# Kernel optimization log

Hardware: AMD Instinct MI355X
Metric: run time of the kernel (lower is better)

## Reference

```python
import jax, jax.numpy as jnp
import numpy as np

B, T, D, H, TE = 8, 1024, 1024, 16, 2048  # batch, seq, latent_dim, heads, time_embed_dim
LN_EPS = 1e-5


def layer_norm(x, w, b):
    m = jnp.mean(x, axis=-1, keepdims=True)
    v = jnp.var(x, axis=-1, keepdims=True)
    return (x - m) / jnp.sqrt(v + LN_EPS) * w + b


def setup_inputs() -> dict:
    key = jax.random.key(0)
    ks = jax.random.split(key, 8)
    s = lambda k, sh: (jax.random.normal(k, sh, jnp.float32) * 0.02)
    return dict(
        x=jax.random.normal(ks[0], (B, T, D), jnp.float32),
        emb=jax.random.normal(ks[1], (B, TE), jnp.float32),
        src_mask=jnp.ones((B, T), jnp.float32),
        norm_w=jnp.ones((D,), jnp.float32), norm_b=jnp.zeros((D,), jnp.float32),
        q_w=s(ks[2], (D, D)), q_b=jnp.zeros((D,), jnp.float32),
        k_w=s(ks[3], (D, D)), k_b=jnp.zeros((D,), jnp.float32),
        v_w=s(ks[4], (D, D)), v_b=jnp.zeros((D,), jnp.float32),
        emb_w=s(ks[5], (TE, 2 * D)), emb_b=jnp.zeros((2 * D,), jnp.float32),
        sb_norm_w=jnp.ones((D,), jnp.float32), sb_norm_b=jnp.zeros((D,), jnp.float32),
        out_w=s(ks[6], (D, D)), out_b=jnp.zeros((D,), jnp.float32),
    )


def reference(x, emb, src_mask, norm_w, norm_b, q_w, q_b, k_w, k_b, v_w, v_b,
              emb_w, emb_b, sb_norm_w, sb_norm_b, out_w, out_b):
    Bx, Tx, Dx = x.shape
    # the torch module applies the SAME LayerNorm to x three times; compute once
    xn = layer_norm(x, norm_w, norm_b)                      # [B,T,D]
    q = (xn @ q_w + q_b).reshape(Bx, Tx, H, -1)             # [B,T,H,l]
    k = (xn @ k_w + k_b).reshape(Bx, Tx, H, -1)
    att = jnp.einsum('bnhl,bmhl->bnmh', q, k)               # [B,T,T,H] (no 1/sqrt(d) scaling, as in source)
    mask = src_mask.reshape(Bx, 1, Tx, 1)
    att = att + (1.0 - mask) * -1000000.0
    att = jax.nn.softmax(att, axis=2)                       # softmax over keys (dim m)
    v = ((xn @ v_w + v_b) * src_mask[:, :, None]).reshape(Bx, Tx, H, -1)
    y = jnp.einsum('bnmh,bmhl->bnhl', att, v).reshape(Bx, Tx, Dx)
    # StylizationBlock (dropout is identity in eval)
    e = jax.nn.silu(emb) @ emb_w + emb_b                    # [B,2D]
    scale, shift = jnp.split(e[:, None, :], 2, axis=2)      # each [B,1,D]
    h = layer_norm(y, sb_norm_w, sb_norm_b) * (1.0 + scale) + shift
    h = jax.nn.silu(h) @ out_w + out_b
    return x + h
```

## Files before the change

### kernel.cpp

```cpp
#include <hip/hip_runtime.h>
#include <cstddef>
#include <cstdint>

#define B_SZ 8
#define T_SEQ 1024
#define D_MODEL 1024
#define NH 16
#define HD 64
#define TE_DIM 2048
#define BT_ROWS 8192

typedef short bf16x8 __attribute__((ext_vector_type(8)));
typedef float f32x4 __attribute__((ext_vector_type(4)));

#define MFMA16(a, b, c) __builtin_amdgcn_mfma_f32_16x16x32_bf16(a, b, c, 0, 0, 0)
#define EXP2(x) __builtin_amdgcn_exp2f(x)

__device__ inline unsigned short f2b(float f) {
  union { float f; unsigned u; } v; v.f = f;
  unsigned r = v.u + 0x7FFF + ((v.u >> 16) & 1);
  return (unsigned short)(r >> 16);
}

__device__ inline float b2f(unsigned short u) {
  union { unsigned u; float f; } v; v.u = ((unsigned)u) << 16; return v.f;
}

__device__ inline unsigned cvtpk(float a, float b) {
  unsigned r;
  asm("v_cvt_pk_bf16_f32 %0, %1, %2" : "=v"(r) : "v"(a), "v"(b));
  return r;
}

__device__ inline void gll16(const void* g, void* l) {
  __builtin_amdgcn_global_load_lds(
      (const __attribute__((address_space(1))) unsigned int*)g,
      (__attribute__((address_space(3))) unsigned int*)l, 16, 0, 0);
}

__global__ __launch_bounds__(256) void ln_kernel(
    const float* __restrict__ x, const float* __restrict__ w,
    const float* __restrict__ b, unsigned short* __restrict__ out)
{
  __shared__ float red[8];
  int row = blockIdx.x;
  int tid = threadIdx.x;
  const float* xr = x + (size_t)row * D_MODEL;
  float4 xv = *(const float4*)&xr[tid * 4];
  float s  = xv.x + xv.y + xv.z + xv.w;
  float ss = xv.x*xv.x + xv.y*xv.y + xv.z*xv.z + xv.w*xv.w;
  #pragma unroll
  for (int off = 32; off; off >>= 1) {
    s  += __shfl_xor(s, off);
    ss += __shfl_xor(ss, off);
  }
  int wv = tid >> 6;
  if ((tid & 63) == 0) { red[wv] = s; red[4 + wv] = ss; }
  __syncthreads();
  s  = red[0] + red[1] + red[2] + red[3];
  ss = red[4] + red[5] + red[6] + red[7];
  float mean = s * (1.f / D_MODEL);
  float var  = ss * (1.f / D_MODEL) - mean * mean;
  float inv  = rsqrtf(var + 1e-5f);
  float4 w4 = *(const float4*)&w[tid * 4];
  float4 b4 = *(const float4*)&b[tid * 4];
  ushort4 o;
  o.x = f2b((xv.x - mean) * inv * w4.x + b4.x);
  o.y = f2b((xv.y - mean) * inv * w4.y + b4.y);
  o.z = f2b((xv.z - mean) * inv * w4.z + b4.z);
  o.w = f2b((xv.w - mean) * inv * w4.w + b4.w);
  int kg = tid >> 4, cb = (tid >> 1) & 7, e = (tid & 1) * 4;
  int col = kg * 64 + ((cb ^ (row & 7)) * 8) + e;
  *(ushort4*)&out[(size_t)row * D_MODEL + col] = o;
}

__global__ __launch_bounds__(256) void transpose_w4(
    const float* __restrict__ s0, const float* __restrict__ s1,
    const float* __restrict__ s2, const float* __restrict__ s3,
    unsigned short* __restrict__ d0, unsigned short* __restrict__ d1,
    unsigned short* __restrict__ d2, unsigned short* __restrict__ d3)
{
  __shared__ float s[32][33];
  int z = blockIdx.z;
  const float* in = z == 0 ? s0 : z == 1 ? s1 : z == 2 ? s2 : s3;
  unsigned short* out = z == 0 ? d0 : z == 1 ? d1 : z == 2 ? d2 : d3;
  int tx = threadIdx.x & 31, ty = threadIdx.x >> 5;
  int r0 = blockIdx.y * 32, c0 = blockIdx.x * 32;
  #pragma unroll
  for (int rr = 0; rr < 4; ++rr)
    s[ty + rr * 8][tx] = in[(size_t)(r0 + ty + rr * 8) * D_MODEL + c0 + tx];
  __syncthreads();
  int k = r0 + tx;
  int kg = k >> 6, cb = (k >> 3) & 7, e = k & 7;
  #pragma unroll
  for (int rr = 0; rr < 4; ++rr) {
    int n = c0 + ty + rr * 8;
    int col = kg * 64 + ((cb ^ (n & 7)) * 8) + e;
    out[(size_t)n * D_MODEL + col] = f2b(s[tx][ty + rr * 8]);
  }
}

__global__ __launch_bounds__(256) void gemm_qkv(
    const unsigned short* __restrict__ A, const unsigned short* __restrict__ W3,
    const float* __restrict__ q_b, const float* __restrict__ k_b,
    const float* __restrict__ v_b, const float* __restrict__ mask,
    unsigned short* __restrict__ O)
{
  const int K = 1024;
  __shared__ __align__(16) unsigned short As[128 * 64];
  __shared__ __align__(16) unsigned short Bs[128 * 64];
  int l = blockIdx.x;
  int xcd = l & 7, ii = l >> 3;
  int mt = xcd * 8 + (ii & 7), nt = ii >> 3;
  int wg = nt >> 3, ntl = nt & 7;
  int m0 = mt * 128, n0 = ntl * 128;
  const unsigned short* Bt = W3 + ((size_t)wg << 20);
  const float* bias = wg == 0 ? q_b : wg == 1 ? k_b : v_b;

  int tid = threadIdx.x;
  int lane = tid & 63, w = tid >> 6;
  int g = lane >> 4, lq = lane & 15;
  int wr = w >> 1, wc = w & 1;
  f32x4 acc[4][4];
  #pragma unroll
  for (int i = 0; i < 4; ++i)
    #pragma unroll
    for (int j = 0; j < 4; ++j)
      acc[i][j] = (f32x4){0.f, 0.f, 0.f, 0.f};

  const unsigned short* aSrc = A + (size_t)(m0 + (tid >> 3)) * K + (tid & 7) * 8;
  const unsigned short* bSrc = Bt + (size_t)(n0 + (tid >> 3)) * K + (tid & 7) * 8;
  char* aDst = (char*)As + tid * 16;
  char* bDst = (char*)Bs + tid * 16;

  for (int k0 = 0; k0 < K; k0 += 64) {
    #pragma unroll
    for (int it = 0; it < 4; ++it) {
      gll16(aSrc + k0 + it * 32 * K, aDst + it * 4096);
      gll16(bSrc + k0 + it * 32 * K, bDst + it * 4096);
    }
    __syncthreads();
    #pragma unroll
    for (int kh = 0; kh < 2; ++kh) {
      bf16x8 af[4], bfr[4];
      #pragma unroll
      for (int i = 0; i < 4; ++i) {
        int ra = wr * 64 + i * 16 + lq;
        af[i] = *(const bf16x8*)((const char*)As + ra * 128 + (((kh * 4 + g) ^ (ra & 7)) * 16));
        int rb = wc * 64 + i * 16 + lq;
        bfr[i] = *(const bf16x8*)((const char*)Bs + rb * 128 + (((kh * 4 + g) ^ (rb & 7)) * 16));
      }
      #pragma unroll
      for (int i = 0; i < 4; ++i)
        #pragma unroll
        for (int j = 0; j < 4; ++j)
          acc[i][j] = MFMA16(af[i], bfr[j], acc[i][j]);
    }
    __syncthreads();
  }

  int colbase = n0 + wc * 64;
  #pragma unroll
  for (int i = 0; i < 4; ++i) {
    int mrow0 = m0 + wr * 64 + i * 16 + g * 4;
    #pragma unroll
    for (int j = 0; j < 4; ++j) {
      int n = colbase + j * 16 + lq;
      float bv = bias[n];
      int h = n >> 6, dd = n & 63;
      if (wg < 2) {
        float scale = wg == 0 ? 1.44269504f : 1.0f;
        unsigned short* Cb = O + ((size_t)wg << 23);
        #pragma unroll
        for (int rr = 0; rr < 4; ++rr) {
          int m = mrow0 + rr;
          int b = m >> 10, t = m & 1023;
          Cb[((size_t)((b * NH + h) * T_SEQ + t)) * HD + dd] = f2b((acc[i][j][rr] + bv) * scale);
        }
      } else {
        unsigned short* Cb = O + ((size_t)2 << 23);
        int b = mrow0 >> 10, t = mrow0 & 1023;
        ushort4 pk;
        unsigned short* pp = (unsigned short*)&pk;
        #pragma unroll
        for (int rr = 0; rr < 4; ++rr)
          pp[rr] = f2b((acc[i][j][rr] + bv) * mask[mrow0 + rr]);
        *(ushort4*)&Cb[((size_t)((b * NH + h) * HD + dd)) * T_SEQ + t] = pk;
      }
    }
  }
}

__global__ __launch_bounds__(256) void gemm_out(
    const unsigned short* __restrict__ A, const unsigned short* __restrict__ Bt,
    const float* __restrict__ bias, const float* __restrict__ resid,
    float* __restrict__ C)
{
  const int K = 1024;
  __shared__ __align__(16) unsigned short As[128 * 64];
  __shared__ __align__(16) unsigned short Bs[128 * 64];
  int l = blockIdx.x;
  int xcd = l & 7, ii = l >> 3;
  int mt = xcd * 8 + (ii & 7), nt = ii >> 3;
  int m0 = mt * 128, n0 = nt * 128;

  int tid = threadIdx.x;
  int lane = tid & 63, w = tid >> 6;
  int g = lane >> 4, lq = lane & 15;
  int wr = w >> 1, wc = w & 1;
  f32x4 acc[4][4];
  #pragma unroll
  for (int i = 0; i < 4; ++i)
    #pragma unroll
    for (int j = 0; j < 4; ++j)
      acc[i][j] = (f32x4){0.f, 0.f, 0.f, 0.f};

  const unsigned short* aSrc = A + (size_t)(m0 + (tid >> 3)) * K + (tid & 7) * 8;
  const unsigned short* bSrc = Bt + (size_t)(n0 + (tid >> 3)) * K + (tid & 7) * 8;
  char* aDst = (char*)As + tid * 16;
  char* bDst = (char*)Bs + tid * 16;

  for (int k0 = 0; k0 < K; k0 += 64) {
    #pragma unroll
    for (int it = 0; it < 4; ++it) {
      gll16(aSrc + k0 + it * 32 * K, aDst + it * 4096);
      gll16(bSrc + k0 + it * 32 * K, bDst + it * 4096);
    }
    __syncthreads();
    #pragma unroll
    for (int kh = 0; kh < 2; ++kh) {
      bf16x8 af[4], bfr[4];
      #pragma unroll
      for (int i = 0; i < 4; ++i) {
        int ra = wr * 64 + i * 16 + lq;
        af[i] = *(const bf16x8*)((const char*)As + ra * 128 + (((kh * 4 + g) ^ (ra & 7)) * 16));
        int rb = wc * 64 + i * 16 + lq;
        bfr[i] = *(const bf16x8*)((const char*)Bs + rb * 128 + (((kh * 4 + g) ^ (rb & 7)) * 16));
      }
      #pragma unroll
      for (int i = 0; i < 4; ++i)
        #pragma unroll
        for (int j = 0; j < 4; ++j)
          acc[i][j] = MFMA16(af[i], bfr[j], acc[i][j]);
    }
    __syncthreads();
  }

  int colbase = n0 + wc * 64;
  #pragma unroll
  for (int i = 0; i < 4; ++i) {
    int mrow0 = m0 + wr * 64 + i * 16 + g * 4;
    #pragma unroll
    for (int j = 0; j < 4; ++j) {
      int n = colbase + j * 16 + lq;
      float bv = bias[n];
      #pragma unroll
      for (int rr = 0; rr < 4; ++rr) {
        int m = mrow0 + rr;
        C[(size_t)m * D_MODEL + n] = acc[i][j][rr] + bv + resid[(size_t)m * D_MODEL + n];
      }
    }
  }
}

__global__ __launch_bounds__(256) void emb_partial(
    const float* __restrict__ emb, const float* __restrict__ emb_w,
    float* __restrict__ partial)
{
  __shared__ float ses[B_SZ][32];
  int tid = threadIdx.x;
  int t0 = blockIdx.y * 32;
  int n = blockIdx.x * 1024 + tid * 4;
  {
    int b = tid >> 5, t = tid & 31;
    float v = emb[b * TE_DIM + t0 + t];
    ses[b][t] = v / (1.f + __expf(-v));
  }
  __syncthreads();
  f32x4 acc[B_SZ];
  #pragma unroll
  for (int b = 0; b < B_SZ; ++b) acc[b] = (f32x4){0.f, 0.f, 0.f, 0.f};
  #pragma unroll 4
  for (int t = 0; t < 32; ++t) {
    f32x4 wv = *(const f32x4*)&emb_w[(size_t)(t0 + t) * (2 * D_MODEL) + n];
    #pragma unroll
    for (int b = 0; b < B_SZ; ++b) {
      float s = ses[b][t];
      acc[b][0] = fmaf(s, wv[0], acc[b][0]);
      acc[b][1] = fmaf(s, wv[1], acc[b][1]);
      acc[b][2] = fmaf(s, wv[2], acc[b][2]);
      acc[b][3] = fmaf(s, wv[3], acc[b][3]);
    }
  }
  #pragma unroll
  for (int b = 0; b < B_SZ; ++b)
    *(f32x4*)&partial[((size_t)blockIdx.y * B_SZ + b) * (2 * D_MODEL) + n] = acc[b];
}

__global__ __launch_bounds__(256) void emb_reduce(
    const float* __restrict__ partial, const float* __restrict__ emb_b,
    float* __restrict__ e)
{
  int idx = blockIdx.x * 256 + threadIdx.x;
  int b = idx >> 11, n = idx & 2047;
  float acc = emb_b[n];
  #pragma unroll 8
  for (int kb = 0; kb < 64; ++kb)
    acc += partial[((size_t)kb * B_SZ + b) * (2 * D_MODEL) + n];
  e[b * (2 * D_MODEL) + n] = acc;
}

__global__ __launch_bounds__(256, 2) void attn_mfma6(
    const unsigned short* __restrict__ Q, const unsigned short* __restrict__ K,
    const unsigned short* __restrict__ Vt, const float* __restrict__ mask,
    unsigned short* __restrict__ y)
{
  __shared__ __align__(16) unsigned short SM[32768];
  unsigned short* Kb = SM;
  unsigned short* Vb = SM + 8192;
  unsigned short* Pb = SM + 16384;

  int tid = threadIdx.x, w = tid >> 6, lane = tid & 63;
  int g = lane >> 4, lq = lane & 15;
  int bid = blockIdx.x;
  int lid = (bid & 7) * 64 + (bid >> 3);
  int qb = lid & 3, h = (lid >> 2) & 15, b = lid >> 6;
  int q0 = qb * 256 + w * 64;
  size_t hb = ((size_t)(b * NH + h)) * T_SEQ * HD;

  bf16x8 bq[4][2];
  #pragma unroll
  for (int qa = 0; qa < 4; ++qa)
    #pragma unroll
    for (int kh = 0; kh < 2; ++kh)
      bq[qa][kh] = *(const bf16x8*)(Q + hb + (size_t)(q0 + qa * 16 + lq) * HD + kh * 32 + g * 8);

  const char* kBase = (const char*)(K + hb) + lq * 128 + g * 16;
  const char* vBase = (const char*)(Vt + hb) + lq * 2048 + g * 16;
  int c0 = 2 * w, c1 = 2 * w + 1;
  const char* kS0 = kBase + (c0 >> 1) * 2048 + (c0 & 1) * 64;
  const char* kS1 = kBase + (c1 >> 1) * 2048 + (c1 & 1) * 64;
  const char* vS0 = vBase + (c0 >> 1) * 32768 + (c0 & 1) * 64;
  const char* vS1 = vBase + (c1 >> 1) * 32768 + (c1 & 1) * 64;

  f32x4 o[4][4];
  #pragma unroll
  for (int dt = 0; dt < 4; ++dt)
    #pragma unroll
    for (int qa = 0; qa < 4; ++qa)
      o[dt][qa] = (f32x4){0.f, 0.f, 0.f, 0.f};
  float mrun[4] = {-3.0e38f, -3.0e38f, -3.0e38f, -3.0e38f};
  float lrun[4] = {0.f, 0.f, 0.f, 0.f};
  const float* maskb = mask + b * T_SEQ;

  gll16(kS0, Kb + c0 * 512);
  gll16(kS1, Kb + c1 * 512);
  gll16(vS0, Vb + c0 * 512);
  gll16(vS1, Vb + c1 * 512);
  __syncthreads();

  for (int t = 0; t < 16; ++t) {
    int cur = t & 1;
    int kv0 = t * 64;
    if (t < 15) {
      int nxt = cur ^ 1;
      size_t ko = (size_t)(kv0 + 64) * 128;
      size_t vo = (size_t)(kv0 + 64) * 2;
      gll16(kS0 + ko, Kb + nxt * 4096 + c0 * 512);
      gll16(kS1 + ko, Kb + nxt * 4096 + c1 * 512);
      gll16(vS0 + vo, Vb + nxt * 4096 + c0 * 512);
      gll16(vS1 + vo, Vb + nxt * 4096 + c1 * 512);
    }
    const unsigned short* Kc = Kb + cur * 4096;
    const unsigned short* Vc = Vb + cur * 4096;

    bf16x8 kf[4][2];
    #pragma unroll
    for (int kt = 0; kt < 4; ++kt)
      #pragma unroll
      for (int kh = 0; kh < 2; ++kh)
        kf[kt][kh] = *(const bf16x8*)(Kc + (kt * 2 + kh) * 512 + lane * 8);

    f32x4 st[4][4];
    #pragma unroll
    for (int kt = 0; kt < 4; ++kt)
      #pragma unroll
      for (int qa = 0; qa < 4; ++qa)
        st[kt][qa] = (f32x4){0.f, 0.f, 0.f, 0.f};

    __builtin_amdgcn_s_setprio(1);
    #pragma unroll
    for (int kt = 0; kt < 4; ++kt)
      #pragma unroll
      for (int qa = 0; qa < 4; ++qa) {
        st[kt][qa] = MFMA16(kf[kt][0], bq[qa][0], st[kt][qa]);
        st[kt][qa] = MFMA16(kf[kt][1], bq[qa][1], st[kt][qa]);
      }
    __builtin_amdgcn_s_setprio(0);

    bf16x8 vf[4][2];
    #pragma unroll
    for (int dt = 0; dt < 4; ++dt)
      #pragma unroll
      for (int kh = 0; kh < 2; ++kh)
        vf[dt][kh] = *(const bf16x8*)(Vc + (dt * 2 + kh) * 512 + lane * 8);

    #pragma unroll
    for (int kt = 0; kt < 4; ++kt) {
      float4 mk = *(const float4*)&maskb[kv0 + kt * 16 + g * 4];
      float mb[4] = {(1.f - mk.x) * -1500000.f, (1.f - mk.y) * -1500000.f,
                     (1.f - mk.z) * -1500000.f, (1.f - mk.w) * -1500000.f};
      #pragma unroll
      for (int qa = 0; qa < 4; ++qa)
        #pragma unroll
        for (int r = 0; r < 4; ++r)
          st[kt][qa][r] += mb[r];
    }

    float tmax[4];
    #pragma unroll
    for (int qa = 0; qa < 4; ++qa) {
      float tm = st[0][qa][0];
      #pragma unroll
      for (int kt = 0; kt < 4; ++kt)
        #pragma unroll
        for (int r = 0; r < 4; ++r)
          tm = fmaxf(tm, st[kt][qa][r]);
      tm = fmaxf(tm, __shfl_xor(tm, 16));
      tm = fmaxf(tm, __shfl_xor(tm, 32));
      tmax[qa] = tm;
    }
    bool need = false;
    #pragma unroll
    for (int qa = 0; qa < 4; ++qa) need = need || (tmax[qa] > mrun[qa] + 11.5f);
    if (__any((int)need)) {
      #pragma unroll
      for (int qa = 0; qa < 4; ++qa) {
        float mnew = fmaxf(mrun[qa], tmax[qa]);
        float corr = EXP2(mrun[qa] - mnew);
        lrun[qa] *= corr;
        #pragma unroll
        for (int dt = 0; dt < 4; ++dt) {
          o[dt][qa][0] *= corr; o[dt][qa][1] *= corr;
          o[dt][qa][2] *= corr; o[dt][qa][3] *= corr;
        }
        mrun[qa] = mnew;
      }
    }
    #pragma unroll
    for (int qa = 0; qa < 4; ++qa) {
      float psum = 0.f;
      #pragma unroll
      for (int kt = 0; kt < 4; ++kt)
        #pragma unroll
        for (int r = 0; r < 4; ++r) {
          float p = EXP2(st[kt][qa][r] - mrun[qa]);
          st[kt][qa][r] = p;
          psum += p;
        }
      psum += __shfl_xor(psum, 16);
      psum += __shfl_xor(psum, 32);
      lrun[qa] += psum;
    }

    #pragma unroll
    for (int qa = 0; qa < 4; ++qa) {
      unsigned short* Pq = Pb + (w * 4 + qa) * 1024;
      #pragma unroll
      for (int kt = 0; kt < 4; ++kt) {
        uint2 pk2;
        pk2.x = cvtpk(st[kt][qa][0], st[kt][qa][1]);
        pk2.y = cvtpk(st[kt][qa][2], st[kt][qa][3]);
        *(uint2*)((char*)Pq + lq * 128 +
                  (((kt * 2 + (g >> 1)) ^ (lq & 7)) * 16) + (g & 1) * 8) = pk2;
      }
    }

    __builtin_amdgcn_s_setprio(1);
    #pragma unroll
    for (int qa = 0; qa < 4; ++qa) {
      const unsigned short* Pq = Pb + (w * 4 + qa) * 1024;
      #pragma unroll
      for (int kh = 0; kh < 2; ++kh) {
        bf16x8 pa = *(const bf16x8*)((const char*)Pq + lq * 128 +
                                     (((kh * 4 + g) ^ (lq & 7)) * 16));
        #pragma unroll
        for (int dt = 0; dt < 4; ++dt)
          o[dt][qa] = MFMA16(vf[dt][kh], pa, o[dt][qa]);
      }
    }
    __builtin_amdgcn_s_setprio(0);

    __syncthreads();
  }

  unsigned short* sc = SM + w * 4096;
  #pragma unroll
  for (int qa = 0; qa < 4; ++qa) {
    float inv = 1.f / lrun[qa];
    #pragma unroll
    for (int dt = 0; dt < 4; ++dt) {
      uint2 pk;
      pk.x = cvtpk(o[dt][qa][0] * inv, o[dt][qa][1] * inv);
      pk.y = cvtpk(o[dt][qa][2] * inv, o[dt][qa][3] * inv);
      *(uint2*)(sc + (qa * 16 + lq) * 64 + dt * 16 + g * 4) = pk;
    }
  }
  #pragma unroll
  for (int it = 0; it < 16; ++it) {
    int row = it * 4 + g;
    ushort4 v = *(const ushort4*)(sc + row * 64 + lq * 4);
    *(ushort4*)&y[(size_t)(b * T_SEQ + q0 + row) * D_MODEL + h * HD + lq * 4] = v;
  }
}

__global__ __launch_bounds__(256) void ln2_kernel(
    const unsigned short* __restrict__ y, const float* __restrict__ w,
    const float* __restrict__ b, const float* __restrict__ e,
    unsigned short* __restrict__ gout)
{
  __shared__ float red[8];
  int row = blockIdx.x;
  int tid = threadIdx.x;
  int bb = row >> 10;
  ushort4 u = *(const ushort4*)&y[(size_t)row * D_MODEL + tid * 4];
  float4 yv = {b2f(u.x), b2f(u.y), b2f(u.z), b2f(u.w)};
  float s  = yv.x + yv.y + yv.z + yv.w;
  float ss = yv.x*yv.x + yv.y*yv.y + yv.z*yv.z + yv.w*yv.w;
  #pragma unroll
  for (int off = 32; off; off >>= 1) {
    s  += __shfl_xor(s, off);
    ss += __shfl_xor(ss, off);
  }
  int wv = tid >> 6;
  if ((tid & 63) == 0) { red[wv] = s; red[4 + wv] = ss; }
  __syncthreads();
  s  = red[0] + red[1] + red[2] + red[3];
  ss = red[4] + red[5] + red[6] + red[7];
  float mean = s * (1.f / D_MODEL);
  float var  = ss * (1.f / D_MODEL) - mean * mean;
  float inv  = rsqrtf(var + 1e-5f);
  float vals[4] = {yv.x, yv.y, yv.z, yv.w};
  ushort4 o;
  unsigned short* op = (unsigned short*)&o;
  #pragma unroll
  for (int j = 0; j < 4; j++) {
    int c = tid * 4 + j;
    float val = (vals[j] - mean) * inv * w[c] + b[c];
    float sc = e[bb * (2 * D_MODEL) + c];
    float sh = e[bb * (2 * D_MODEL) + D_MODEL + c];
    val = val * (1.f + sc) + sh;
    op[j] = f2b(val / (1.f + __expf(-val)));
  }
  int kg = tid >> 4, cb = (tid >> 1) & 7, ee = (tid & 1) * 4;
  int col = kg * 64 + ((cb ^ (row & 7)) * 8) + ee;
  *(ushort4*)&gout[(size_t)row * D_MODEL + col] = o;
}

extern "C" void kernel_launch(void* const* d_in, const int* in_sizes, int n_in,
                              void* d_out, int out_size, void* d_ws, size_t ws_size,
                              hipStream_t stream) {
  const float* x      = (const float*)d_in[0];
  const float* emb    = (const float*)d_in[1];
  const float* mask   = (const float*)d_in[2];
  const float* norm_w = (const float*)d_in[3];
  const float* norm_b = (const float*)d_in[4];
  const float* q_w    = (const float*)d_in[5];
  const float* q_b    = (const float*)d_in[6];
  const float* k_w    = (const float*)d_in[7];
  const float* k_b    = (const float*)d_in[8];
  const float* v_w    = (const float*)d_in[9];
  const float* v_b    = (const float*)d_in[10];
  const float* emb_w  = (const float*)d_in[11];
  const float* emb_b  = (const float*)d_in[12];
  const float* sb_w   = (const float*)d_in[13];
  const float* sb_b   = (const float*)d_in[14];
  const float* out_w  = (const float*)d_in[15];
  const float* out_b  = (const float*)d_in[16];
  float* out = (float*)d_out;

  char* ws = (char*)d_ws;
  const size_t MB = 1u << 20;
  unsigned short* xn   = (unsigned short*)(ws);
  unsigned short* qkv  = (unsigned short*)(ws + 16 * MB);
  unsigned short* qb   = qkv;
  unsigned short* kb   = qkv + (1u << 23);
  unsigned short* vt   = qkv + (2u << 23);
  unsigned short* yb   = (unsigned short*)(ws + 64 * MB);
  unsigned short* gb   = (unsigned short*)(ws + 96 * MB);
  float*          ep   = (float*)(ws + 96 * MB);
  unsigned short* w3t  = (unsigned short*)(ws + 112 * MB);
  unsigned short* owt  = (unsigned short*)(ws + 118 * MB);
  float*          eb   = (float*)(ws + 120 * MB);

  transpose_w4<<<dim3(32, 32, 4), 256, 0, stream>>>(
      q_w, k_w, v_w, out_w,
      w3t, w3t + (1u << 20), w3t + (2u << 20), owt);

  ln_kernel<<<BT_ROWS, 256, 0, stream>>>(x, norm_w, norm_b, xn);

  gemm_qkv<<<1536, 256, 0, stream>>>(xn, w3t, q_b, k_b, v_b, mask, qkv);

  emb_partial<<<dim3(2, 64), 256, 0, stream>>>(emb, emb_w, ep);
  emb_reduce<<<64, 256, 0, stream>>>(ep, emb_b, eb);

  attn_mfma6<<<512, 256, 0, stream>>>(qb, kb, vt, mask, yb);

  ln2_kernel<<<BT_ROWS, 256, 0, stream>>>(yb, sb_w, sb_b, eb, gb);

  gemm_out<<<512, 256, 0, stream>>>(gb, owt, out_b, x, out);
}
```

Before: 192.6 us.

## Unify GEMMs into 256x128-tile triple-buffered 8-wave kernel with async prefetch

Replaces the two single-buffered 128x128 GEMM kernels with one templated kernel that uses 512 threads, 256x128 output tiles and a three-slot shared-memory ring. Loads for tile t+2 are issued before computing tile t, with explicit vmcnt waits and a single barrier per K step, and MFMA sections run at raised wave priority. This is meant to hide global-load latency behind MFMA work and halve the barriers per K step. The cost is about 144KB of LDS per block, which may limit occupancy, and fewer blocks in the grid (768 and 256), which may leave some CUs idle on the smaller GEMM.

```diff
diff --git a/kernel.cpp b/kernel.cpp
--- a/kernel.cpp
+++ b/kernel.cpp
@@ -100,27 +100,28 @@
   }
 }
 
-__global__ __launch_bounds__(256) void gemm_qkv(
-    const unsigned short* __restrict__ A, const unsigned short* __restrict__ W3,
-    const float* __restrict__ q_b, const float* __restrict__ k_b,
-    const float* __restrict__ v_b, const float* __restrict__ mask,
-    unsigned short* __restrict__ O)
+template <int MODE>
+__global__ __launch_bounds__(512, 2) void gemm8(
+    const unsigned short* __restrict__ A, const unsigned short* __restrict__ W,
+    const float* __restrict__ b0, const float* __restrict__ b1,
+    const float* __restrict__ b2, const float* __restrict__ mask,
+    const float* __restrict__ resid, void* __restrict__ C)
 {
   const int K = 1024;
-  __shared__ __align__(16) unsigned short As[128 * 64];
-  __shared__ __align__(16) unsigned short Bs[128 * 64];
-  int l = blockIdx.x;
-  int xcd = l & 7, ii = l >> 3;
-  int mt = xcd * 8 + (ii & 7), nt = ii >> 3;
-  int wg = nt >> 3, ntl = nt & 7;
-  int m0 = mt * 128, n0 = ntl * 128;
-  const unsigned short* Bt = W3 + ((size_t)wg << 20);
-  const float* bias = wg == 0 ? q_b : wg == 1 ? k_b : v_b;
-
+  __shared__ __align__(16) unsigned short SA[3][256 * 64];
+  __shared__ __align__(16) unsigned short SB[3][128 * 64];
   int tid = threadIdx.x;
-  int lane = tid & 63, w = tid >> 6;
-  int g = lane >> 4, lq = lane & 15;
-  int wr = w >> 1, wc = w & 1;
+  int wid = tid >> 6, lane = tid & 63, g = lane >> 4, lq = lane & 15;
+  int wm = wid >> 1, wn = wid & 1;
+  int bid = blockIdx.x;
+  int xcd = bid & 7, ii = bid >> 3;
+  int mt = xcd * 4 + (ii & 3), nt = ii >> 2;
+  int m0 = mt * 256;
+  int wg = (MODE == 1) ? (nt >> 3) : 0;
+  int n0 = (MODE == 1) ? ((nt & 7) * 128) : (nt * 128);
+  const unsigned short* Bt = W + ((size_t)wg << 20);
+  const float* bias = (MODE == 1) ? (wg == 0 ? b0 : wg == 1 ? b1 : b2) : b0;
+
   f32x4 acc[4][4];
   #pragma unroll
   for (int i = 0; i < 4; ++i)
@@ -130,134 +131,98 @@
 
   const unsigned short* aSrc = A + (size_t)(m0 + (tid >> 3)) * K + (tid & 7) * 8;
   const unsigned short* bSrc = Bt + (size_t)(n0 + (tid >> 3)) * K + (tid & 7) * 8;
-  char* aDst = (char*)As + tid * 16;
-  char* bDst = (char*)Bs + tid * 16;
-
-  for (int k0 = 0; k0 < K; k0 += 64) {
-    #pragma unroll
-    for (int it = 0; it < 4; ++it) {
-      gll16(aSrc + k0 + it * 32 * K, aDst + it * 4096);
-      gll16(bSrc + k0 + it * 32 * K, bDst + it * 4096);
-    }
-    __syncthreads();
-    #pragma unroll
-    for (int kh = 0; kh < 2; ++kh) {
-      bf16x8 af[4], bfr[4];
-      #pragma unroll
-      for (int i = 0; i < 4; ++i) {
-        int ra = wr * 64 + i * 16 + lq;
-        af[i] = *(const bf16x8*)((const char*)As + ra * 128 + (((kh * 4 + g) ^ (ra & 7)) * 16));
-        int rb = wc * 64 + i * 16 + lq;
-        bfr[i] = *(const bf16x8*)((const char*)Bs + rb * 128 + (((kh * 4 + g) ^ (rb & 7)) * 16));
+
+  #define STAGE8(slot, t)                                                      \
+    {                                                                          \
+      size_t ko = (size_t)(t) * 64;                                            \
+      _Pragma("unroll")                                                        \
+      for (int i2 = 0; i2 < 4; ++i2)                                           \
+        gll16(aSrc + ko + (size_t)i2 * 64 * K,                                 \
+              (char*)&SA[slot][0] + tid * 16 + i2 * 8192);                     \
+      _Pragma("unroll")                                                        \
+      for (int i2 = 0; i2 < 2; ++i2)                                           \
+        gll16(bSrc + ko + (size_t)i2 * 64 * K,                                 \
+              (char*)&SB[slot][0] + tid * 16 + i2 * 8192);                     \
+    }
+
+  STAGE8(0, 0)
+  STAGE8(1, 1)
+  asm volatile("s_waitcnt vmcnt(6)" ::: "memory");
+  asm volatile("s_barrier" ::: "memory");
+
+  int cA0 = (g ^ (lq & 7)) * 16;
+  int cA1 = ((4 + g) ^ (lq & 7)) * 16;
+
+  #pragma unroll
+  for (int t = 0; t < 16; ++t) {
+    const char* sa = (const char*)&SA[t % 3][0];
+    const char* sb = (const char*)&SB[t % 3][0];
+    bf16x8 af[4][2], bf[4][2];
+    #pragma unroll
+    for (int i = 0; i < 4; ++i) {
+      int ra = wm * 64 + i * 16 + lq;
+      af[i][0] = *(const bf16x8*)(sa + ra * 128 + cA0);
+      af[i][1] = *(const bf16x8*)(sa + ra * 128 + cA1);
+      int rb = wn * 64 + i * 16 + lq;
+      bf[i][0] = *(const bf16x8*)(sb + rb * 128 + cA0);
+      bf[i][1] = *(const bf16x8*)(sb + rb * 128 + cA1);
+    }
+    if (t < 14) {
+      STAGE8((t + 2) % 3, t + 2)
+      asm volatile("s_waitcnt vmcnt(6)" ::: "memory");
+    } else if (t == 14) {
+      asm volatile("s_waitcnt vmcnt(0)" ::: "memory");
+    }
+    __builtin_amdgcn_s_setprio(1);
+    #pragma unroll
+    for (int i = 0; i < 4; ++i)
+      #pragma unroll
+      for (int j = 0; j < 4; ++j) {
+        acc[i][j] = MFMA16(af[i][0], bf[j][0], acc[i][j]);
+        acc[i][j] = MFMA16(af[i][1], bf[j][1], acc[i][j]);
       }
-      #pragma unroll
-      for (int i = 0; i < 4; ++i)
-        #pragma unroll
-        for (int j = 0; j < 4; ++j)
-          acc[i][j] = MFMA16(af[i], bfr[j], acc[i][j]);
-    }
-    __syncthreads();
-  }
-
-  int colbase = n0 + wc * 64;
+    __builtin_amdgcn_s_setprio(0);
+    if (t < 15) asm volatile("s_barrier" ::: "memory");
+  }
+  #undef STAGE8
+
+  int colbase = n0 + wn * 64;
   #pragma unroll
   for (int i = 0; i < 4; ++i) {
-    int mrow0 = m0 + wr * 64 + i * 16 + g * 4;
+    int mrow0 = m0 + wm * 64 + i * 16 + g * 4;
     #pragma unroll
     for (int j = 0; j < 4; ++j) {
       int n = colbase + j * 16 + lq;
       float bv = bias[n];
-      int h = n >> 6, dd = n & 63;
-      if (wg < 2) {
-        float scale = wg == 0 ? 1.44269504f : 1.0f;
-        unsigned short* Cb = O + ((size_t)wg << 23);
+      if (MODE == 0) {
+        float* Cf = (float*)C;
         #pragma unroll
         for (int rr = 0; rr < 4; ++rr) {
           int m = mrow0 + rr;
-          int b = m >> 10, t = m & 1023;
-          Cb[((size_t)((b * NH + h) * T_SEQ + t)) * HD + dd] = f2b((acc[i][j][rr] + bv) * scale);
+          Cf[(size_t)m * D_MODEL + n] = acc[i][j][rr] + bv + resid[(size_t)m * D_MODEL + n];
         }
       } else {
-        unsigned short* Cb = O + ((size_t)2 << 23);
-        int b = mrow0 >> 10, t = mrow0 & 1023;
-        ushort4 pk;
-        unsigned short* pp = (unsigned short*)&pk;
-        #pragma unroll
-        for (int rr = 0; rr < 4; ++rr)
-          pp[rr] = f2b((acc[i][j][rr] + bv) * mask[mrow0 + rr]);
-        *(ushort4*)&Cb[((size_t)((b * NH + h) * HD + dd)) * T_SEQ + t] = pk;
-      }
-    }
-  }
-}
-
-__global__ __launch_bounds__(256) void gemm_out(
-    const unsigned short* __restrict__ A, const unsigned short* __restrict__ Bt,
-    const float* __restrict__ bias, const float* __restrict__ resid,
-    float* __restrict__ C)
-{
-  const int K = 1024;
-  __shared__ __align__(16) unsigned short As[128 * 64];
-  __shared__ __align__(16) unsigned short Bs[128 * 64];
-  int l = blockIdx.x;
-  int xcd = l & 7, ii = l >> 3;
-  int mt = xcd * 8 + (ii & 7), nt = ii >> 3;
-  int m0 = mt * 128, n0 = nt * 128;
-
-  int tid = threadIdx.x;
-  int lane = tid & 63, w = tid >> 6;
-  int g = lane >> 4, lq = lane & 15;
-  int wr = w >> 1, wc = w & 1;
-  f32x4 acc[4][4];
-  #pragma unroll
-  for (int i = 0; i < 4; ++i)
-    #pragma unroll
-    for (int j = 0; j < 4; ++j)
-      acc[i][j] = (f32x4){0.f, 0.f, 0.f, 0.f};
-
-  const unsigned short* aSrc = A + (size_t)(m0 + (tid >> 3)) * K + (tid & 7) * 8;
-  const unsigned short* bSrc = Bt + (size_t)(n0 + (tid >> 3)) * K + (tid & 7) * 8;
-  char* aDst = (char*)As + tid * 16;
-  char* bDst = (char*)Bs + tid * 16;
-
-  for (int k0 = 0; k0 < K; k0 += 64) {
-    #pragma unroll
-    for (int it = 0; it < 4; ++it) {
-      gll16(aSrc + k0 + it * 32 * K, aDst + it * 4096);
-      gll16(bSrc + k0 + it * 32 * K, bDst + it * 4096);
-    }
-    __syncthreads();
-    #pragma unroll
-    for (int kh = 0; kh < 2; ++kh) {
-      bf16x8 af[4], bfr[4];
-      #pragma unroll
-      for (int i = 0; i < 4; ++i) {
-        int ra = wr * 64 + i * 16 + lq;
-        af[i] = *(const bf16x8*)((const char*)As + ra * 128 + (((kh * 4 + g) ^ (ra & 7)) * 16));
-        int rb = wc * 64 + i * 16 + lq;
-        bfr[i] = *(const bf16x8*)((const char*)Bs + rb * 128 + (((kh * 4 + g) ^ (rb & 7)) * 16));
-      }
-      #pragma unroll
-      for (int i = 0; i < 4; ++i)
-        #pragma unroll
-        for (int j = 0; j < 4; ++j)
-          acc[i][j] = MFMA16(af[i], bfr[j], acc[i][j]);
-    }
-    __syncthreads();
-  }
-
-  int colbase = n0 + wc * 64;
-  #pragma unroll
-  for (int i = 0; i < 4; ++i) {
-    int mrow0 = m0 + wr * 64 + i * 16 + g * 4;
-    #pragma unroll
-    for (int j = 0; j < 4; ++j) {
-      int n = colbase + j * 16 + lq;
-      float bv = bias[n];
-      #pragma unroll
-      for (int rr = 0; rr < 4; ++rr) {
-        int m = mrow0 + rr;
-        C[(size_t)m * D_MODEL + n] = acc[i][j][rr] + bv + resid[(size_t)m * D_MODEL + n];
+        int h = n >> 6, dd = n & 63;
+        unsigned short* O = (unsigned short*)C;
+        if (wg < 2) {
+          float scale = wg == 0 ? 1.44269504f : 1.0f;
+          unsigned short* Cb = O + ((size_t)wg << 23);
+          #pragma unroll
+          for (int rr = 0; rr < 4; ++rr) {
+            int m = mrow0 + rr;
+            int b = m >> 10, tt = m & 1023;
+            Cb[((size_t)((b * NH + h) * T_SEQ + tt)) * HD + dd] = f2b((acc[i][j][rr] + bv) * scale);
+          }
+        } else {
+          unsigned short* Cb = O + ((size_t)2 << 23);
+          int b = mrow0 >> 10, tt = mrow0 & 1023;
+          ushort4 pk;
+          unsigned short* pp = (unsigned short*)&pk;
+          #pragma unroll
+          for (int rr = 0; rr < 4; ++rr)
+            pp[rr] = f2b((acc[i][j][rr] + bv) * mask[mrow0 + rr]);
+          *(ushort4*)&Cb[((size_t)((b * NH + h) * HD + dd)) * T_SEQ + tt] = pk;
+        }
       }
     }
   }
@@ -599,7 +564,7 @@
 
   ln_kernel<<<BT_ROWS, 256, 0, stream>>>(x, norm_w, norm_b, xn);
 
-  gemm_qkv<<<1536, 256, 0, stream>>>(xn, w3t, q_b, k_b, v_b, mask, qkv);
+  gemm8<1><<<768, 512, 0, stream>>>(xn, w3t, q_b, k_b, v_b, mask, nullptr, qkv);
 
   emb_partial<<<dim3(2, 64), 256, 0, stream>>>(emb, emb_w, ep);
   emb_reduce<<<64, 256, 0, stream>>>(ep, emb_b, eb);
@@ -608,5 +573,5 @@
 
   ln2_kernel<<<BT_ROWS, 256, 0, stream>>>(yb, sb_w, sb_b, eb, gb);
 
-  gemm_out<<<512, 256, 0, stream>>>(gb, owt, out_b, x, out);
-}
+  gemm8<0><<<256, 512, 0, stream>>>(gb, owt, out_b, nullptr, nullptr, nullptr, x, out);
+}
```

After: 200.9 us. +4.3%, slower.
